# Performance work log

Measured on AMD Instinct MI355X. Metric: run time of the kernel, lower is better.

Reference implementation:

```python
import jax, jax.numpy as jnp
import numpy as np

N = 50000
E = 800000
IN = 128
H = 128
R = 8
OUT = 2
BN_EPS = 1e-5


def setup_inputs() -> dict:
    key = jax.random.key(0)
    ks = jax.random.split(key, 16)
    s1 = 1.0 / np.sqrt(IN)
    s2 = 1.0 / np.sqrt(H)
    return {
        "x": jax.random.normal(ks[0], (N, IN), dtype=jnp.float32),
        "edge_index": jax.random.randint(ks[1], (2, E), 0, N, dtype=jnp.int32),
        "edge_type": jax.random.randint(ks[2], (E,), 0, R, dtype=jnp.int32),
        # layer 1 RGCNConv params
        "w1": jax.random.normal(ks[3], (R, IN, H), dtype=jnp.float32) * s1,
        "root1": jax.random.normal(ks[4], (IN, H), dtype=jnp.float32) * s1,
        "b1": jnp.zeros((H,), dtype=jnp.float32),
        "g1": jnp.ones((H,), dtype=jnp.float32),
        "be1": jnp.zeros((H,), dtype=jnp.float32),
        # layer 2 RGCNConv params
        "w2": jax.random.normal(ks[5], (R, H, H), dtype=jnp.float32) * s2,
        "root2": jax.random.normal(ks[6], (H, H), dtype=jnp.float32) * s2,
        "b2": jnp.zeros((H,), dtype=jnp.float32),
        "g2": jnp.ones((H,), dtype=jnp.float32),
        "be2": jnp.zeros((H,), dtype=jnp.float32),
        # classifier
        "cw": jax.random.normal(ks[7], (H, OUT), dtype=jnp.float32) * s2,
        "cb": jnp.zeros((OUT,), dtype=jnp.float32),
    }


def rgcn_conv(x, src, tgt, et, W, root, b):
    """PyG-style RGCNConv with per-relation mean aggregation.

    out[v] = sum_r mean_{e: tgt=v, type=r} (x[src_e] @ W[r]) + x[v] @ root + b
    """
    n = x.shape[0]
    # per-(node, relation) in-degree for mean normalization
    comp = tgt * R + et  # composite segment id, [E]
    deg = jax.ops.segment_sum(jnp.ones_like(et, dtype=x.dtype), comp,
                              num_segments=n * R)
    inv_deg = jnp.where(deg > 0, 1.0 / jnp.maximum(deg, 1.0), 0.0)
    # transform every node by every relation weight: [n, R, out]
    xw = jnp.einsum('ni,rio->nro', x, W)
    # gather per-edge message and apply mean normalization: [E, out]
    msg = xw[src, et] * inv_deg[comp][:, None]
    agg = jax.ops.segment_sum(msg, tgt, num_segments=n)
    return agg + x @ root + b


def batchnorm(x, gamma, beta):
    # training-mode BatchNorm1d over node dim (biased variance, eps=1e-5)
    mean = jnp.mean(x, axis=0)
    var = jnp.mean(jnp.square(x - mean), axis=0)
    return gamma * (x - mean) * jax.lax.rsqrt(var + BN_EPS) + beta


def reference(x, edge_index, edge_type, w1, root1, b1, g1, be1,
              w2, root2, b2, g2, be2, cw, cb):
    src, tgt = edge_index[0], edge_index[1]
    h = rgcn_conv(x, src, tgt, edge_type, w1, root1, b1)
    h = jax.nn.relu(batchnorm(h, g1, be1))
    h = rgcn_conv(h, src, tgt, edge_type, w2, root2, b2)
    h = jax.nn.relu(batchnorm(h, g2, be2))
    return h @ cw + cb
```

## Files before the change

### kernel.cpp

```cpp
#include <hip/hip_runtime.h>
#include <hip/hip_bf16.h>

#define N_NODES 50000
#define N_EDGES 800000
#define DIM 128
#define NREL 8
#define KTOT 1152
#define NRSEG (N_NODES * NREL)
#define BN_EPS 1e-5f

typedef __attribute__((ext_vector_type(8))) short bf16x8;
typedef __attribute__((ext_vector_type(16))) float f32x16;

__device__ inline float b2f(short s) {
    union { unsigned u; float f; } t;
    t.u = ((unsigned)(unsigned short)s) << 16;
    return t.f;
}
__device__ inline short f2b(float f) {
    __hip_bfloat16 h = __float2bfloat16(f);
    return *reinterpret_cast<short*>(&h);
}


__global__ void k_hist(const int* __restrict__ ei, const int* __restrict__ et,
                       int* __restrict__ cnt) {
    int e = blockIdx.x * 256 + threadIdx.x;
    if (e < N_EDGES) {
        int tgt = ei[N_EDGES + e];
        int r = et[e];
        atomicAdd(&cnt[tgt * NREL + r], 1);
    }
}

__global__ void k_alloc(const int* __restrict__ cnt, int* __restrict__ offs,
                        int* __restrict__ cursor) {
    int i = blockIdx.x * 256 + threadIdx.x;
    int lane = threadIdx.x & 63;
    int c = (i < NRSEG) ? cnt[i] : 0;
    int incl = c;
    #pragma unroll
    for (int d = 1; d < 64; d <<= 1) {
        int t = __shfl_up(incl, d, 64);
        if (lane >= d) incl += t;
    }
    int total = __shfl(incl, 63, 64);
    int base = 0;
    if (lane == 63) base = atomicAdd(cursor, total);
    base = __shfl(base, 63, 64);
    if (i < NRSEG) offs[i] = base + incl - c;
}

__global__ void k_fill(const int* __restrict__ ei, const int* __restrict__ et,
                       const int* __restrict__ offs, int* __restrict__ fillcur,
                       int* __restrict__ sorted) {
    int e = blockIdx.x * 256 + threadIdx.x;
    if (e < N_EDGES) {
        int src = ei[e];
        int tgt = ei[N_EDGES + e];
        int comp = tgt * NREL + et[e];
        int pos = atomicAdd(&fillcur[comp], 1);
        sorted[offs[comp] + pos] = src;
    }
}

__global__ void k_wconv(const float* __restrict__ W, const float* __restrict__ root,
                        __hip_bfloat16* __restrict__ Bt) {
    int idx = blockIdx.x * 256 + threadIdx.x;
    if (idx >= DIM * KTOT) return;
    int o = idx / KTOT, k = idx % KTOT;
    float v;
    if (k < NREL * DIM) {
        int r = k >> 7, i = k & 127;
        v = W[(r * DIM + i) * DIM + o];
    } else {
        int i = k - NREL * DIM;
        v = root[i * DIM + o];
    }
    Bt[idx] = __float2bfloat16(v);
}

__global__ void k_cast(const float* __restrict__ in, __hip_bfloat16* __restrict__ out) {
    int i = (blockIdx.x * 256 + threadIdx.x) * 4;
    if (i >= N_NODES * DIM) return;
    float4 v = *(const float4*)&in[i];
    short4 o;
    o.x = f2b(v.x); o.y = f2b(v.y); o.z = f2b(v.z); o.w = f2b(v.w);
    *(short4*)&out[i] = o;
}

__global__ void k_cast2(const __hip_bfloat16* __restrict__ in, const float* __restrict__ bn,
                        __hip_bfloat16* __restrict__ out) {
    int i = (blockIdx.x * 256 + threadIdx.x) * 8;
    if (i >= N_NODES * DIM) return;
    bf16x8 v = *(const bf16x8*)&in[i];
    int ch = i & 127;
    bf16x8 o;
    #pragma unroll
    for (int j = 0; j < 8; ++j) {
        float f = b2f(v[j]);
        f = fmaxf(f * bn[ch + j] + bn[128 + ch + j], 0.f);
        o[j] = f2b(f);
    }
    *(bf16x8*)&out[i] = o;
}

__global__ __launch_bounds__(256) void k_fused(
        const __hip_bfloat16* __restrict__ xb,
        const int* __restrict__ cnt, const int* __restrict__ offs,
        const int* __restrict__ sorted,
        const __hip_bfloat16* __restrict__ Bt,
        const float* __restrict__ bias,
        __hip_bfloat16* __restrict__ h, float* __restrict__ stats) {
    __shared__ __hip_bfloat16 At[64 * 128];
    int tid = threadIdx.x;
    int n0 = blockIdx.x * 64;
    int g = tid >> 4, il = tid & 15;
    int lane = tid & 63, wid = tid >> 6;
    int half = lane >> 5, l31 = lane & 31;
    int rbase = (wid & 1) * 32, cbase = (wid >> 1) * 64;

    const __hip_bfloat16* bBase0 = Bt + (size_t)(cbase + l31) * KTOT + half * 8;
    const __hip_bfloat16* bBase1 = Bt + (size_t)(cbase + 32 + l31) * KTOT + half * 8;

    f32x16 acc0 = {}, acc1 = {};

    for (int r = 0; r < 9; ++r) {
        if (r < 8) {
            int c4[4], o4[4];
            float s4[4][8];
            #pragma unroll
            for (int s = 0; s < 4; ++s) {
                int node = n0 + g + s * 16;
                bool ok = node < N_NODES;
                int comp = node * NREL + r;
                c4[s] = ok ? cnt[comp] : 0;
                o4[s] = ok ? offs[comp] : 0;
                #pragma unroll
                for (int j = 0; j < 8; ++j) s4[s][j] = 0.f;
            }
            int mx = max(max(c4[0], c4[1]), max(c4[2], c4[3]));
            for (int i = 0; i < mx; ++i) {
                #pragma unroll
                for (int s = 0; s < 4; ++s) {
                    if (i < c4[s]) {
                        int idx = sorted[o4[s] + i];
                        bf16x8 rv = *(const bf16x8*)&xb[(size_t)idx * DIM + il * 8];
                        #pragma unroll
                        for (int j = 0; j < 8; ++j) s4[s][j] += b2f(rv[j]);
                    }
                }
            }
            #pragma unroll
            for (int s = 0; s < 4; ++s) {
                int vi = g + s * 16;
                float inv = (c4[s] > 0) ? 1.f / (float)c4[s] : 0.f;
                bf16x8 ov;
                #pragma unroll
                for (int j = 0; j < 8; ++j) ov[j] = f2b(s4[s][j] * inv);
                int slot = il ^ (vi & 15);
                *(bf16x8*)&At[vi * 128 + slot * 8] = ov;
            }
        } else {
            #pragma unroll
            for (int s = 0; s < 4; ++s) {
                int vi = g + s * 16;
                int node = n0 + vi;
                bf16x8 rv = {};
                if (node < N_NODES) rv = *(const bf16x8*)&xb[(size_t)node * DIM + il * 8];
                int slot = il ^ (vi & 15);
                *(bf16x8*)&At[vi * 128 + slot * 8] = rv;
            }
        }
        __syncthreads();
        const __hip_bfloat16* b0 = bBase0 + r * DIM;
        const __hip_bfloat16* b1 = bBase1 + r * DIM;
        int arow = rbase + l31;
        #pragma unroll
        for (int ks = 0; ks < 8; ++ks) {
            int slot = (2 * ks + half) ^ (arow & 15);
            bf16x8 a = *(const bf16x8*)&At[arow * 128 + slot * 8];
            bf16x8 f0 = *(const bf16x8*)(b0 + ks * 16);
            bf16x8 f1 = *(const bf16x8*)(b1 + ks * 16);
            acc0 = __builtin_amdgcn_mfma_f32_32x32x16_bf16(a, f0, acc0, 0, 0, 0);
            acc1 = __builtin_amdgcn_mfma_f32_32x32x16_bf16(a, f1, acc1, 0, 0, 0);
        }
        __syncthreads();
    }

    float bv0 = bias[cbase + l31];
    float bv1 = bias[cbase + 32 + l31];
    float s1a = 0.f, s2a = 0.f, s1b = 0.f, s2b = 0.f;
    #pragma unroll
    for (int reg = 0; reg < 16; ++reg) {
        int row = n0 + rbase + (reg & 3) + 8 * (reg >> 2) + 4 * half;
        float v0 = acc0[reg] + bv0;
        float v1 = acc1[reg] + bv1;
        if (row < N_NODES) {
            h[(size_t)row * DIM + cbase + l31] = __float2bfloat16(v0);
            h[(size_t)row * DIM + cbase + 32 + l31] = __float2bfloat16(v1);
            s1a += v0; s2a += v0 * v0;
            s1b += v1; s2b += v1 * v1;
        }
    }
    s1a += __shfl_xor(s1a, 32, 64); s2a += __shfl_xor(s2a, 32, 64);
    s1b += __shfl_xor(s1b, 32, 64); s2b += __shfl_xor(s2b, 32, 64);
    if (half == 0) {
        atomicAdd(&stats[cbase + l31], s1a);
        atomicAdd(&stats[128 + cbase + l31], s2a);
        atomicAdd(&stats[cbase + 32 + l31], s1b);
        atomicAdd(&stats[128 + cbase + 32 + l31], s2b);
    }
}

__global__ void k_bnfinal(const float* __restrict__ stats, const float* __restrict__ g,
                          const float* __restrict__ be, float* __restrict__ bn) {
    int c = threadIdx.x;
    float mean = stats[c] / (float)N_NODES;
    float var = stats[128 + c] / (float)N_NODES - mean * mean;
    float a = g[c] * rsqrtf(var + BN_EPS);
    bn[c] = a;
    bn[128 + c] = be[c] - mean * a;
}

__global__ void k_classifier(const __hip_bfloat16* __restrict__ h, const float* __restrict__ bn,
                             const float* __restrict__ cw, const float* __restrict__ cb,
                             float* __restrict__ out) {
    int w = blockIdx.x * 4 + (threadIdx.x >> 6);
    int lane = threadIdx.x & 63;
    if (w >= N_NODES) return;
    int c = lane * 2;
    __hip_bfloat162 hv = *(const __hip_bfloat162*)&h[(size_t)w * DIM + c];
    float x0 = __bfloat162float(hv.x), x1 = __bfloat162float(hv.y);
    float p0 = fmaxf(x0 * bn[c] + bn[128 + c], 0.f);
    float p1 = fmaxf(x1 * bn[c + 1] + bn[128 + c + 1], 0.f);
    float acc0 = p0 * cw[c * 2] + p1 * cw[(c + 1) * 2];
    float acc1 = p0 * cw[c * 2 + 1] + p1 * cw[(c + 1) * 2 + 1];
    #pragma unroll
    for (int d = 32; d; d >>= 1) {
        acc0 += __shfl_down(acc0, d, 64);
        acc1 += __shfl_down(acc1, d, 64);
    }
    if (lane == 0) {
        out[w * 2] = acc0 + cb[0];
        out[w * 2 + 1] = acc1 + cb[1];
    }
}

extern "C" void kernel_launch(void* const* d_in, const int* in_sizes, int n_in,
                              void* d_out, int out_size, void* d_ws, size_t ws_size,
                              hipStream_t stream) {
    const float* x    = (const float*)d_in[0];
    const int*   ei   = (const int*)d_in[1];
    const int*   et   = (const int*)d_in[2];
    const float* w1   = (const float*)d_in[3];
    const float* root1= (const float*)d_in[4];
    const float* b1   = (const float*)d_in[5];
    const float* g1   = (const float*)d_in[6];
    const float* be1  = (const float*)d_in[7];
    const float* w2   = (const float*)d_in[8];
    const float* root2= (const float*)d_in[9];
    const float* b2   = (const float*)d_in[10];
    const float* g2   = (const float*)d_in[11];
    const float* be2  = (const float*)d_in[12];
    const float* cw   = (const float*)d_in[13];
    const float* cb   = (const float*)d_in[14];
    float* out = (float*)d_out;

    char* ws = (char*)d_ws;
    size_t off = 0;
    auto alloc = [&](size_t bytes) -> char* {
        char* p = ws + off;
        off += (bytes + 255) & ~(size_t)255;
        return p;
    };
    int*   cnt     = (int*)alloc((size_t)NRSEG * 4);
    int*   fillcur = (int*)alloc((size_t)NRSEG * 4);
    int*   cursor  = (int*)alloc(256);
    float* stats1  = (float*)alloc(1024);
    float* stats2  = (float*)alloc(1024);
    size_t zero_bytes = off;
    int*   offs    = (int*)alloc((size_t)NRSEG * 4);
    float* bn1     = (float*)alloc(1024);
    float* bn2     = (float*)alloc(1024);
    __hip_bfloat16* Bt1 = (__hip_bfloat16*)alloc((size_t)DIM * KTOT * 2);
    __hip_bfloat16* Bt2 = (__hip_bfloat16*)alloc((size_t)DIM * KTOT * 2);
    int*   sorted  = (int*)alloc((size_t)N_EDGES * 4);
    __hip_bfloat16* h1 = (__hip_bfloat16*)alloc((size_t)N_NODES * DIM * 2);
    __hip_bfloat16* h2 = (__hip_bfloat16*)alloc((size_t)N_NODES * DIM * 2);
    __hip_bfloat16* xb = (__hip_bfloat16*)alloc((size_t)N_NODES * DIM * 2);

    hipMemsetAsync(d_ws, 0, zero_bytes, stream);

    k_hist<<<(N_EDGES + 255) / 256, 256, 0, stream>>>(ei, et, cnt);
    k_alloc<<<(NRSEG + 255) / 256, 256, 0, stream>>>(cnt, offs, cursor);
    k_fill<<<(N_EDGES + 255) / 256, 256, 0, stream>>>(ei, et, offs, fillcur, sorted);
    k_wconv<<<(DIM * KTOT + 255) / 256, 256, 0, stream>>>(w1, root1, Bt1);
    k_wconv<<<(DIM * KTOT + 255) / 256, 256, 0, stream>>>(w2, root2, Bt2);

    int fused_grid = (N_NODES + 63) / 64;

    k_cast<<<(N_NODES * DIM / 4 + 255) / 256, 256, 0, stream>>>(x, xb);
    k_fused<<<fused_grid, 256, 0, stream>>>(xb, cnt, offs, sorted, Bt1, b1, h1, stats1);
    k_bnfinal<<<1, 128, 0, stream>>>(stats1, g1, be1, bn1);

    k_cast2<<<(N_NODES * DIM / 8 + 255) / 256, 256, 0, stream>>>(h1, bn1, xb);
    k_fused<<<fused_grid, 256, 0, stream>>>(xb, cnt, offs, sorted, Bt2, b2, h2, stats2);
    k_bnfinal<<<1, 128, 0, stream>>>(stats2, g2, be2, bn2);

    k_classifier<<<(N_NODES + 3) / 4, 256, 0, stream>>>(h2, bn2, cw, cb, out);
}
```

Before: 604.7 us.

## Gather all relations up front then run one MFMA pass per 32-node tile

The fused RGCN kernel now gathers the mean-aggregated neighbor features for all 8 relations plus the root features into a 32x1152 shared tile before any matrix math. This replaces the nine gather/sync/MFMA phases of the old 64-node kernel. Each thread now works on 8 relations at once, so more independent gather loads are in flight and 16 barriers collapse into one. Tiles shrink to 32 nodes, each wave computes one 32-column slice, and the kernel requests 2 blocks per CU. In exchange it uses more registers (8x8 float accumulators) and more shared memory, and per-relation degree imbalance inside one thread can lengthen its loop to the maximum count across relations.

```diff
diff --git a/kernel.cpp b/kernel.cpp
--- a/kernel.cpp
+++ b/kernel.cpp
@@ -8,6 +8,7 @@
 #define KTOT 1152
 #define NRSEG (N_NODES * NREL)
 #define BN_EPS 1e-5f
+#define ATSTRIDE 1160
 
 typedef __attribute__((ext_vector_type(8))) short bf16x8;
 typedef __attribute__((ext_vector_type(16))) float f32x16;
@@ -105,111 +106,103 @@
     *(bf16x8*)&out[i] = o;
 }
 
-__global__ __launch_bounds__(256) void k_fused(
+__global__ __launch_bounds__(256, 2) void k_fused2(
         const __hip_bfloat16* __restrict__ xb,
         const int* __restrict__ cnt, const int* __restrict__ offs,
         const int* __restrict__ sorted,
         const __hip_bfloat16* __restrict__ Bt,
         const float* __restrict__ bias,
         __hip_bfloat16* __restrict__ h, float* __restrict__ stats) {
-    __shared__ __hip_bfloat16 At[64 * 128];
+    __shared__ __hip_bfloat16 At[32 * ATSTRIDE];
     int tid = threadIdx.x;
-    int n0 = blockIdx.x * 64;
-    int g = tid >> 4, il = tid & 15;
+    int n0 = blockIdx.x * 32;
+    int unit = tid >> 4, il = tid & 15;
+    int ubase = (tid & 63) & 48;
+
+    #pragma unroll 1
+    for (int rr = 0; rr < 2; ++rr) {
+        int vi = unit + rr * 16;
+        int node = n0 + vi;
+        bool ok = node < N_NODES;
+        int c = 0, o = 0;
+        if (ok && il < 8) {
+            c = cnt[node * NREL + il];
+            o = offs[node * NREL + il];
+        }
+        int c8[8], o8[8];
+        #pragma unroll
+        for (int r = 0; r < 8; ++r) {
+            c8[r] = __shfl(c, ubase + r, 64);
+            o8[r] = __shfl(o, ubase + r, 64);
+        }
+        int mx = 0;
+        #pragma unroll
+        for (int r = 0; r < 8; ++r) mx = max(mx, c8[r]);
+
+        float s[8][8];
+        #pragma unroll
+        for (int r = 0; r < 8; ++r)
+            #pragma unroll
+            for (int j = 0; j < 8; ++j) s[r][j] = 0.f;
+
+        for (int i = 0; i < mx; ++i) {
+            #pragma unroll
+            for (int r = 0; r < 8; ++r) {
+                if (i < c8[r]) {
+                    int idx = sorted[o8[r] + i];
+                    bf16x8 rv = *(const bf16x8*)&xb[(size_t)idx * DIM + il * 8];
+                    #pragma unroll
+                    for (int j = 0; j < 8; ++j) s[r][j] += b2f(rv[j]);
+                }
+            }
+        }
+        #pragma unroll
+        for (int r = 0; r < 8; ++r) {
+            float inv = (c8[r] > 0) ? 1.f / (float)c8[r] : 0.f;
+            bf16x8 ov;
+            #pragma unroll
+            for (int j = 0; j < 8; ++j) ov[j] = f2b(s[r][j] * inv);
+            *(bf16x8*)&At[vi * ATSTRIDE + r * DIM + il * 8] = ov;
+        }
+        bf16x8 sv = {};
+        if (ok) sv = *(const bf16x8*)&xb[(size_t)node * DIM + il * 8];
+        *(bf16x8*)&At[vi * ATSTRIDE + NREL * DIM + il * 8] = sv;
+    }
+
+    __syncthreads();
+
     int lane = tid & 63, wid = tid >> 6;
     int half = lane >> 5, l31 = lane & 31;
-    int rbase = (wid & 1) * 32, cbase = (wid >> 1) * 64;
-
-    const __hip_bfloat16* bBase0 = Bt + (size_t)(cbase + l31) * KTOT + half * 8;
-    const __hip_bfloat16* bBase1 = Bt + (size_t)(cbase + 32 + l31) * KTOT + half * 8;
-
-    f32x16 acc0 = {}, acc1 = {};
-
+    const __hip_bfloat16* bBase = Bt + (size_t)(wid * 32 + l31) * KTOT + half * 8;
+    const __hip_bfloat16* aBase = &At[l31 * ATSTRIDE + half * 8];
+    f32x16 acc = {};
+    #pragma unroll
     for (int r = 0; r < 9; ++r) {
-        if (r < 8) {
-            int c4[4], o4[4];
-            float s4[4][8];
-            #pragma unroll
-            for (int s = 0; s < 4; ++s) {
-                int node = n0 + g + s * 16;
-                bool ok = node < N_NODES;
-                int comp = node * NREL + r;
-                c4[s] = ok ? cnt[comp] : 0;
-                o4[s] = ok ? offs[comp] : 0;
-                #pragma unroll
-                for (int j = 0; j < 8; ++j) s4[s][j] = 0.f;
-            }
-            int mx = max(max(c4[0], c4[1]), max(c4[2], c4[3]));
-            for (int i = 0; i < mx; ++i) {
-                #pragma unroll
-                for (int s = 0; s < 4; ++s) {
-                    if (i < c4[s]) {
-                        int idx = sorted[o4[s] + i];
-                        bf16x8 rv = *(const bf16x8*)&xb[(size_t)idx * DIM + il * 8];
-                        #pragma unroll
-                        for (int j = 0; j < 8; ++j) s4[s][j] += b2f(rv[j]);
-                    }
-                }
-            }
-            #pragma unroll
-            for (int s = 0; s < 4; ++s) {
-                int vi = g + s * 16;
-                float inv = (c4[s] > 0) ? 1.f / (float)c4[s] : 0.f;
-                bf16x8 ov;
-                #pragma unroll
-                for (int j = 0; j < 8; ++j) ov[j] = f2b(s4[s][j] * inv);
-                int slot = il ^ (vi & 15);
-                *(bf16x8*)&At[vi * 128 + slot * 8] = ov;
-            }
-        } else {
-            #pragma unroll
-            for (int s = 0; s < 4; ++s) {
-                int vi = g + s * 16;
-                int node = n0 + vi;
-                bf16x8 rv = {};
-                if (node < N_NODES) rv = *(const bf16x8*)&xb[(size_t)node * DIM + il * 8];
-                int slot = il ^ (vi & 15);
-                *(bf16x8*)&At[vi * 128 + slot * 8] = rv;
-            }
-        }
-        __syncthreads();
-        const __hip_bfloat16* b0 = bBase0 + r * DIM;
-        const __hip_bfloat16* b1 = bBase1 + r * DIM;
-        int arow = rbase + l31;
         #pragma unroll
         for (int ks = 0; ks < 8; ++ks) {
-            int slot = (2 * ks + half) ^ (arow & 15);
-            bf16x8 a = *(const bf16x8*)&At[arow * 128 + slot * 8];
-            bf16x8 f0 = *(const bf16x8*)(b0 + ks * 16);
-            bf16x8 f1 = *(const bf16x8*)(b1 + ks * 16);
-            acc0 = __builtin_amdgcn_mfma_f32_32x32x16_bf16(a, f0, acc0, 0, 0, 0);
-            acc1 = __builtin_amdgcn_mfma_f32_32x32x16_bf16(a, f1, acc1, 0, 0, 0);
-        }
-        __syncthreads();
-    }
-
-    float bv0 = bias[cbase + l31];
-    float bv1 = bias[cbase + 32 + l31];
-    float s1a = 0.f, s2a = 0.f, s1b = 0.f, s2b = 0.f;
+            bf16x8 a = *(const bf16x8*)(aBase + r * DIM + ks * 16);
+            bf16x8 b = *(const bf16x8*)(bBase + r * DIM + ks * 16);
+            acc = __builtin_amdgcn_mfma_f32_32x32x16_bf16(a, b, acc, 0, 0, 0);
+        }
+    }
+
+    int col = wid * 32 + l31;
+    float bv = bias[col];
+    float s1 = 0.f, s2 = 0.f;
     #pragma unroll
     for (int reg = 0; reg < 16; ++reg) {
-        int row = n0 + rbase + (reg & 3) + 8 * (reg >> 2) + 4 * half;
-        float v0 = acc0[reg] + bv0;
-        float v1 = acc1[reg] + bv1;
+        int row = n0 + (reg & 3) + 8 * (reg >> 2) + 4 * half;
+        float v = acc[reg] + bv;
         if (row < N_NODES) {
-            h[(size_t)row * DIM + cbase + l31] = __float2bfloat16(v0);
-            h[(size_t)row * DIM + cbase + 32 + l31] = __float2bfloat16(v1);
-            s1a += v0; s2a += v0 * v0;
-            s1b += v1; s2b += v1 * v1;
-        }
-    }
-    s1a += __shfl_xor(s1a, 32, 64); s2a += __shfl_xor(s2a, 32, 64);
-    s1b += __shfl_xor(s1b, 32, 64); s2b += __shfl_xor(s2b, 32, 64);
+            h[(size_t)row * DIM + col] = __float2bfloat16(v);
+            s1 += v; s2 += v * v;
+        }
+    }
+    s1 += __shfl_xor(s1, 32, 64);
+    s2 += __shfl_xor(s2, 32, 64);
     if (half == 0) {
-        atomicAdd(&stats[cbase + l31], s1a);
-        atomicAdd(&stats[128 + cbase + l31], s2a);
-        atomicAdd(&stats[cbase + 32 + l31], s1b);
-        atomicAdd(&stats[128 + cbase + 32 + l31], s2b);
+        atomicAdd(&stats[col], s1);
+        atomicAdd(&stats[128 + col], s2);
     }
 }
 
@@ -298,14 +291,14 @@
     k_wconv<<<(DIM * KTOT + 255) / 256, 256, 0, stream>>>(w1, root1, Bt1);
     k_wconv<<<(DIM * KTOT + 255) / 256, 256, 0, stream>>>(w2, root2, Bt2);
 
-    int fused_grid = (N_NODES + 63) / 64;
+    int fused_grid = (N_NODES + 31) / 32;
 
     k_cast<<<(N_NODES * DIM / 4 + 255) / 256, 256, 0, stream>>>(x, xb);
-    k_fused<<<fused_grid, 256, 0, stream>>>(xb, cnt, offs, sorted, Bt1, b1, h1, stats1);
+    k_fused2<<<fused_grid, 256, 0, stream>>>(xb, cnt, offs, sorted, Bt1, b1, h1, stats1);
     k_bnfinal<<<1, 128, 0, stream>>>(stats1, g1, be1, bn1);
 
     k_cast2<<<(N_NODES * DIM / 8 + 255) / 256, 256, 0, stream>>>(h1, bn1, xb);
-    k_fused<<<fused_grid, 256, 0, stream>>>(xb, cnt, offs, sorted, Bt2, b2, h2, stats2);
+    k_fused2<<<fused_grid, 256, 0, stream>>>(xb, cnt, offs, sorted, Bt2, b2, h2, stats2);
     k_bnfinal<<<1, 128, 0, stream>>>(stats2, g2, be2, bn2);
 
     k_classifier<<<(N_NODES + 3) / 4, 256, 0, stream>>>(h2, bn2, cw, cb, out);
```

Result: slower. 699.5 us (+15.7%).
